# Kernel tuning notes

Hardware: AMD Instinct MI355X
Metric: run time of the kernel (lower is better)

Reference implementation:

```python
import jax, jax.numpy as jnp
import numpy as np

N_POINTS = 2_000_000
N_VOXELS = 1_500_000
N_SP = 50_000
C = 32
LN_EPS = 1e-5  # torch nn.LayerNorm default


def setup_inputs() -> dict:
    key = jax.random.key(0)
    ks = jax.random.split(key, 8)
    voxel_feats = jax.random.normal(ks[0], (N_VOXELS, C), jnp.float32)
    xyz = jax.random.normal(ks[1], (N_POINTS, 3), jnp.float32)
    p2v_map = jax.random.randint(ks[2], (N_POINTS,), 0, N_VOXELS, dtype=jnp.int32)
    sp_ids = jax.random.randint(ks[3], (N_POINTS,), 0, N_SP, dtype=jnp.int32)
    W1 = jax.random.normal(ks[4], (3, C), jnp.float32) * (1.0 / np.sqrt(3.0))
    b1 = jnp.zeros((C,), jnp.float32)
    gamma = jnp.ones((C,), jnp.float32)
    beta = jnp.zeros((C,), jnp.float32)
    W2 = jax.random.normal(ks[5], (C, C), jnp.float32) * (1.0 / np.sqrt(C))
    b2 = jnp.zeros((C,), jnp.float32)
    return {
        'voxel_feats': voxel_feats, 'xyz': xyz,
        'W1': W1, 'b1': b1, 'gamma': gamma, 'beta': beta, 'W2': W2, 'b2': b2,
        'p2v_map': p2v_map, 'sp_ids': sp_ids, 'num_superpoints': N_SP,
    }


def reference(voxel_feats, xyz, W1, b1, gamma, beta, W2, b2, p2v_map, sp_ids, num_superpoints):
    # gather voxel features to points: x = voxel_feats[p2v_map]  [N_pts, C]
    x = voxel_feats[p2v_map]

    # pos_encode MLP: Linear(3,32) -> LayerNorm(32) -> ReLU -> Linear(32,32)
    h = xyz @ W1 + b1
    mu = jnp.mean(h, axis=-1, keepdims=True)
    var = jnp.mean(jnp.square(h - mu), axis=-1, keepdims=True)
    h = (h - mu) * jax.lax.rsqrt(var + LN_EPS) * gamma + beta
    x_pos = jax.nn.relu(h) @ W2 + b2

    # scatter(reduce='mean') into superpoints; compute counts once
    counts = jax.ops.segment_sum(jnp.ones((xyz.shape[0],), x.dtype), sp_ids,
                                 num_segments=num_superpoints)
    denom = jnp.maximum(counts, 1.0)[:, None]

    def smean(v):
        return jax.ops.segment_sum(v, sp_ids, num_segments=num_superpoints) / denom

    x_sp = smean(x) + smean(x_pos)          # [S, C]
    sp_xyz = smean(xyz)                      # [S, 3]
    return (x_sp, sp_xyz)
```

## Files before the change

kernel.cpp:

```cpp
#include <hip/hip_runtime.h>
#include <hip/hip_bf16.h>

#define C 32
#define LN_EPS 1e-5f
#define P 8
#define SCAN_BLK 1024

__global__ __launch_bounds__(256) void k1_hist_rank(
    const int* __restrict__ sp_ids, int* __restrict__ count,
    int* __restrict__ rank, int n)
{
    int p = blockIdx.x * 256 + threadIdx.x;
    if (p >= n) return;
    int sp = sp_ids[p];
    rank[p] = atomicAdd(&count[sp], 1);
}

__global__ __launch_bounds__(SCAN_BLK) void k2a_scan_block(
    const int* __restrict__ count, int* __restrict__ off,
    int* __restrict__ bsum, int S)
{
    __shared__ int lds[SCAN_BLK];
    int t = threadIdx.x;
    int i = blockIdx.x * SCAN_BLK + t;
    int v = (i < S) ? count[i] : 0;
    lds[t] = v;
    __syncthreads();
    for (int d = 1; d < SCAN_BLK; d <<= 1) {
        int add = (t >= d) ? lds[t - d] : 0;
        __syncthreads();
        lds[t] += add;
        __syncthreads();
    }
    int incl = lds[t];
    if (i < S) off[i] = incl - v;
    if (t == SCAN_BLK - 1) bsum[blockIdx.x] = incl;
}

__global__ __launch_bounds__(64) void k2b_scan_bsums(int* __restrict__ bsum, int nb)
{
    int lane = threadIdx.x;
    int v = (lane < nb) ? bsum[lane] : 0;
    int own = v;
    for (int d = 1; d < 64; d <<= 1) {
        int u = __shfl_up(v, d, 64);
        if (lane >= d) v += u;
    }
    if (lane < nb) bsum[lane] = v - own;
}

__global__ __launch_bounds__(256) void k2c_add_prefix(
    int* __restrict__ off, const int* __restrict__ bsum, int S)
{
    int i = blockIdx.x * 256 + threadIdx.x;
    if (i >= S) return;
    off[i] += bsum[i / SCAN_BLK];
}

__global__ __launch_bounds__(256) void kA_mlp_scatter(
    const float* __restrict__ voxel_feats,
    const float* __restrict__ xyz,
    const float* __restrict__ W1, const float* __restrict__ b1,
    const float* __restrict__ gamma, const float* __restrict__ beta,
    const float* __restrict__ W2, const float* __restrict__ b2,
    const int* __restrict__ p2v, const int* __restrict__ sp_ids,
    const int* __restrict__ rank, const int* __restrict__ off,
    unsigned int* __restrict__ y_s,
    float* __restrict__ xyz_s,
    int n)
{
    int p = blockIdx.x * 256 + threadIdx.x;
    if (p >= n) return;

    float x0 = xyz[3 * p + 0];
    float x1 = xyz[3 * p + 1];
    float x2 = xyz[3 * p + 2];
    int v  = p2v[p];
    int sp = sp_ids[p];
    int j  = off[sp] + rank[p];

    float h[C];
    #pragma unroll
    for (int c = 0; c < C; ++c)
        h[c] = fmaf(x0, W1[c], fmaf(x1, W1[C + c], fmaf(x2, W1[2 * C + c], b1[c])));

    float s = 0.f, s2 = 0.f;
    #pragma unroll
    for (int c = 0; c < C; ++c) { s += h[c]; s2 += h[c] * h[c]; }
    float mu   = s * (1.0f / C);
    float var  = fmaf(-mu, mu, s2 * (1.0f / C));
    float rstd = rsqrtf(var + LN_EPS);

    #pragma unroll
    for (int c = 0; c < C; ++c)
        h[c] = fmaxf(fmaf((h[c] - mu) * rstd, gamma[c], beta[c]), 0.0f);

    float acc[C];
    const float4* vf4 = (const float4*)(voxel_feats + (size_t)v * C);
    #pragma unroll
    for (int q = 0; q < 8; ++q) {
        float4 f = vf4[q];
        acc[4 * q + 0] = b2[4 * q + 0] + f.x;
        acc[4 * q + 1] = b2[4 * q + 1] + f.y;
        acc[4 * q + 2] = b2[4 * q + 2] + f.z;
        acc[4 * q + 3] = b2[4 * q + 3] + f.w;
    }
    #pragma unroll
    for (int k = 0; k < C; ++k) {
        float rk = h[k];
        #pragma unroll
        for (int c = 0; c < C; ++c)
            acc[c] = fmaf(rk, W2[k * C + c], acc[c]);
    }

    unsigned int w[16];
    #pragma unroll
    for (int q = 0; q < 16; ++q) {
        __hip_bfloat162 bb = __float22bfloat162_rn(make_float2(acc[2 * q], acc[2 * q + 1]));
        w[q] = *reinterpret_cast<unsigned int*>(&bb);
    }
    uint4* dst = (uint4*)(y_s + (size_t)j * 16);
    dst[0] = make_uint4(w[0], w[1], w[2], w[3]);
    dst[1] = make_uint4(w[4], w[5], w[6], w[7]);
    dst[2] = make_uint4(w[8], w[9], w[10], w[11]);
    dst[3] = make_uint4(w[12], w[13], w[14], w[15]);

    float* xd = xyz_s + (size_t)j * 3;
    xd[0] = x0; xd[1] = x1; xd[2] = x2;
}

__global__ __launch_bounds__(256) void kB_reduce(
    const unsigned int* __restrict__ y_s,
    const float* __restrict__ xyz_s,
    const int* __restrict__ off, const int* __restrict__ count,
    float* __restrict__ out_x,
    float* __restrict__ out_xyz,
    int S)
{
    int gt  = blockIdx.x * 256 + threadIdx.x;
    int sp  = gt >> 3;
    int sub = gt & 7;
    if (sp >= S) return;

    int n    = count[sp];
    int base = off[sp];

    float acc[C];
    #pragma unroll
    for (int c = 0; c < C; ++c) acc[c] = 0.f;
    float ax = 0.f, ay = 0.f, az = 0.f;

    for (int i = sub; i < n; i += P) {
        const uint4* r4 = (const uint4*)(y_s + (size_t)(base + i) * 16);
        unsigned int w[16];
        *(uint4*)(w + 0)  = r4[0];
        *(uint4*)(w + 4)  = r4[1];
        *(uint4*)(w + 8)  = r4[2];
        *(uint4*)(w + 12) = r4[3];
        #pragma unroll
        for (int q = 0; q < 16; ++q) {
            acc[2 * q + 0] += __uint_as_float(w[q] << 16);
            acc[2 * q + 1] += __uint_as_float(w[q] & 0xFFFF0000u);
        }
        const float* xp = xyz_s + (size_t)(base + i) * 3;
        ax += xp[0]; ay += xp[1]; az += xp[2];
    }

    #pragma unroll
    for (int c = 0; c < C; ++c) {
        acc[c] += __shfl_xor(acc[c], 1);
        acc[c] += __shfl_xor(acc[c], 2);
        acc[c] += __shfl_xor(acc[c], 4);
    }
    ax += __shfl_xor(ax, 1); ax += __shfl_xor(ax, 2); ax += __shfl_xor(ax, 4);
    ay += __shfl_xor(ay, 1); ay += __shfl_xor(ay, 2); ay += __shfl_xor(ay, 4);
    az += __shfl_xor(az, 1); az += __shfl_xor(az, 2); az += __shfl_xor(az, 4);

    if (sub == 0) {
        float inv = 1.0f / fmaxf((float)n, 1.0f);
        float4* o4 = (float4*)(out_x + (size_t)sp * C);
        #pragma unroll
        for (int q = 0; q < 8; ++q) {
            float4 f;
            f.x = acc[4 * q + 0] * inv;
            f.y = acc[4 * q + 1] * inv;
            f.z = acc[4 * q + 2] * inv;
            f.w = acc[4 * q + 3] * inv;
            o4[q] = f;
        }
        out_xyz[3 * sp + 0] = ax * inv;
        out_xyz[3 * sp + 1] = ay * inv;
        out_xyz[3 * sp + 2] = az * inv;
    }
}

__global__ __launch_bounds__(256) void k3_reorder(
    const int* __restrict__ sp_ids, const int* __restrict__ rank,
    const int* __restrict__ off, int* __restrict__ order, int n)
{
    int p = blockIdx.x * 256 + threadIdx.x;
    if (p >= n) return;
    int sp = sp_ids[p];
    order[off[sp] + rank[p]] = p;
}

__global__ __launch_bounds__(256) void k4_segment_mlp_mean(
    const float* __restrict__ voxel_feats, const float* __restrict__ xyz,
    const float* __restrict__ W1, const float* __restrict__ b1,
    const float* __restrict__ gamma, const float* __restrict__ beta,
    const float* __restrict__ W2, const float* __restrict__ b2,
    const int* __restrict__ p2v, const int* __restrict__ order,
    const int* __restrict__ off, const int* __restrict__ count,
    float* __restrict__ out_x, float* __restrict__ out_xyz, int S)
{
    int gt  = blockIdx.x * 256 + threadIdx.x;
    int sp  = gt >> 3;
    int sub = gt & 7;
    if (sp >= S) return;

    int n    = count[sp];
    int base = off[sp];

    float acc[C];
    #pragma unroll
    for (int c = 0; c < C; ++c) acc[c] = 0.f;
    float ax = 0.f, ay = 0.f, az = 0.f;
    int my_pts = 0;

    for (int i = sub; i < n; i += P) {
        int p = order[base + i];
        float x0 = xyz[3 * p + 0];
        float x1 = xyz[3 * p + 1];
        float x2 = xyz[3 * p + 2];
        int v = p2v[p];

        float h[C];
        #pragma unroll
        for (int c = 0; c < C; ++c)
            h[c] = fmaf(x0, W1[c], fmaf(x1, W1[C + c], fmaf(x2, W1[2 * C + c], b1[c])));
        float s = 0.f, s2 = 0.f;
        #pragma unroll
        for (int c = 0; c < C; ++c) { s += h[c]; s2 += h[c] * h[c]; }
        float mu   = s * (1.0f / C);
        float var  = fmaf(-mu, mu, s2 * (1.0f / C));
        float rstd = rsqrtf(var + LN_EPS);
        #pragma unroll
        for (int c = 0; c < C; ++c)
            h[c] = fmaxf(fmaf((h[c] - mu) * rstd, gamma[c], beta[c]), 0.0f);

        const float4* vf4 = (const float4*)(voxel_feats + (size_t)v * C);
        #pragma unroll
        for (int q = 0; q < 8; ++q) {
            float4 f = vf4[q];
            acc[4 * q + 0] += f.x;
            acc[4 * q + 1] += f.y;
            acc[4 * q + 2] += f.z;
            acc[4 * q + 3] += f.w;
        }
        #pragma unroll
        for (int k = 0; k < C; ++k) {
            float rk = h[k];
            #pragma unroll
            for (int c = 0; c < C; ++c)
                acc[c] = fmaf(rk, W2[k * C + c], acc[c]);
        }
        ax += x0; ay += x1; az += x2;
        ++my_pts;
    }

    float fpts = (float)my_pts;
    #pragma unroll
    for (int c = 0; c < C; ++c) acc[c] = fmaf(fpts, b2[c], acc[c]);

    #pragma unroll
    for (int c = 0; c < C; ++c) {
        acc[c] += __shfl_xor(acc[c], 1);
        acc[c] += __shfl_xor(acc[c], 2);
        acc[c] += __shfl_xor(acc[c], 4);
    }
    ax += __shfl_xor(ax, 1); ax += __shfl_xor(ax, 2); ax += __shfl_xor(ax, 4);
    ay += __shfl_xor(ay, 1); ay += __shfl_xor(ay, 2); ay += __shfl_xor(ay, 4);
    az += __shfl_xor(az, 1); az += __shfl_xor(az, 2); az += __shfl_xor(az, 4);

    if (sub == 0) {
        float inv = 1.0f / fmaxf((float)n, 1.0f);
        float4* o4 = (float4*)(out_x + (size_t)sp * C);
        #pragma unroll
        for (int q = 0; q < 8; ++q) {
            float4 f;
            f.x = acc[4 * q + 0] * inv;
            f.y = acc[4 * q + 1] * inv;
            f.z = acc[4 * q + 2] * inv;
            f.w = acc[4 * q + 3] * inv;
            o4[q] = f;
        }
        out_xyz[3 * sp + 0] = ax * inv;
        out_xyz[3 * sp + 1] = ay * inv;
        out_xyz[3 * sp + 2] = az * inv;
    }
}

extern "C" void kernel_launch(void* const* d_in, const int* in_sizes, int n_in,
                              void* d_out, int out_size, void* d_ws, size_t ws_size,
                              hipStream_t stream)
{
    const float* voxel_feats = (const float*)d_in[0];
    const float* xyz         = (const float*)d_in[1];
    const float* W1          = (const float*)d_in[2];
    const float* b1          = (const float*)d_in[3];
    const float* gamma       = (const float*)d_in[4];
    const float* beta        = (const float*)d_in[5];
    const float* W2          = (const float*)d_in[6];
    const float* b2          = (const float*)d_in[7];
    const int*   p2v         = (const int*)d_in[8];
    const int*   sp_ids      = (const int*)d_in[9];

    const int n_pts = in_sizes[8];
    const int S     = out_size / 35;

    float* out_x   = (float*)d_out;
    float* out_xyz = out_x + (size_t)S * C;

    int* count = (int*)d_ws;
    int* off   = count + S;
    int* bsum  = off + S;
    int* rank  = bsum + 64;

    size_t head_bytes = ((size_t)2 * S + 64 + (size_t)n_pts) * sizeof(int);
    size_t needA = head_bytes + (size_t)n_pts * 64 + (size_t)n_pts * 12;

    int blk = 256;
    int gpts = (n_pts + blk - 1) / blk;
    int nb = (S + SCAN_BLK - 1) / SCAN_BLK;

    hipMemsetAsync(count, 0, (size_t)S * sizeof(int), stream);
    k1_hist_rank<<<gpts, blk, 0, stream>>>(sp_ids, count, rank, n_pts);
    k2a_scan_block<<<nb, SCAN_BLK, 0, stream>>>(count, off, bsum, S);
    k2b_scan_bsums<<<1, 64, 0, stream>>>(bsum, nb);
    k2c_add_prefix<<<(S + blk - 1) / blk, blk, 0, stream>>>(off, bsum, S);

    int n_thr = S * P;
    if (ws_size >= needA) {
        unsigned int* y_s = (unsigned int*)((char*)d_ws + head_bytes);
        float* xyz_s = (float*)((char*)d_ws + head_bytes + (size_t)n_pts * 64);

        kA_mlp_scatter<<<gpts, blk, 0, stream>>>(
            voxel_feats, xyz, W1, b1, gamma, beta, W2, b2,
            p2v, sp_ids, rank, off, y_s, xyz_s, n_pts);
        kB_reduce<<<(n_thr + blk - 1) / blk, blk, 0, stream>>>(
            y_s, xyz_s, off, count, out_x, out_xyz, S);
    } else {
        int* order = rank + n_pts;
        k3_reorder<<<gpts, blk, 0, stream>>>(sp_ids, rank, off, order, n_pts);
        k4_segment_mlp_mean<<<(n_thr + blk - 1) / blk, blk, 0, stream>>>(
            voxel_feats, xyz, W1, b1, gamma, beta, W2, b2,
            p2v, order, off, count, out_x, out_xyz, S);
    }
}
```

Baseline: 578.9 us.

## Pre-convert voxel features to bf16 and pack per-point records into aligned 128B slots

Adds a fused histogram/rank kernel that also converts voxel features to bf16 into workspace, so the per-point MLP kernel gathers half-size voxel rows. Per-point outputs and xyz are packed into one 128-byte aligned record, and each thread processes two points. The intent is to cut gather traffic and get full-line aligned writes. The trade-off is an extra full pass over the voxel table, zero padding that adds write bytes, and extra bf16 rounding of the input features.

```diff
diff --git a/kernel.cpp b/kernel.cpp
--- a/kernel.cpp
+++ b/kernel.cpp
@@ -5,6 +5,34 @@
 #define LN_EPS 1e-5f
 #define P 8
 #define SCAN_BLK 1024
+
+__device__ __forceinline__ unsigned pack_bf16x2(float a, float b) {
+    __hip_bfloat162 bb = __float22bfloat162_rn(make_float2(a, b));
+    return *reinterpret_cast<unsigned*>(&bb);
+}
+
+__global__ __launch_bounds__(256) void kVk1(
+    const int* __restrict__ sp_ids, int* __restrict__ count, int* __restrict__ rank,
+    const float* __restrict__ vf, unsigned* __restrict__ vf16,
+    int n_pts, int n_chunk)
+{
+    int t = blockIdx.x * 256 + threadIdx.x;
+    if (t < n_pts) {
+        int sp = sp_ids[t];
+        rank[t] = atomicAdd(&count[sp], 1);
+    }
+    if (t < n_chunk) {
+        const float4* src = (const float4*)vf + (size_t)t * 4;
+        float4 a = src[0], b = src[1], c = src[2], d = src[3];
+        uint4 o0, o1;
+        o0.x = pack_bf16x2(a.x, a.y); o0.y = pack_bf16x2(a.z, a.w);
+        o0.z = pack_bf16x2(b.x, b.y); o0.w = pack_bf16x2(b.z, b.w);
+        o1.x = pack_bf16x2(c.x, c.y); o1.y = pack_bf16x2(c.z, c.w);
+        o1.z = pack_bf16x2(d.x, d.y); o1.w = pack_bf16x2(d.z, d.w);
+        uint4* dst = (uint4*)vf16 + (size_t)t * 2;
+        dst[0] = o0; dst[1] = o1;
+    }
+}
 
 __global__ __launch_bounds__(256) void k1_hist_rank(
     const int* __restrict__ sp_ids, int* __restrict__ count,
@@ -57,85 +85,97 @@
     off[i] += bsum[i / SCAN_BLK];
 }
 
-__global__ __launch_bounds__(256) void kA_mlp_scatter(
-    const float* __restrict__ voxel_feats,
+template<bool BF16VF>
+__global__ __launch_bounds__(256) void kA_rec(
+    const void* __restrict__ vfeats,
     const float* __restrict__ xyz,
     const float* __restrict__ W1, const float* __restrict__ b1,
     const float* __restrict__ gamma, const float* __restrict__ beta,
     const float* __restrict__ W2, const float* __restrict__ b2,
     const int* __restrict__ p2v, const int* __restrict__ sp_ids,
     const int* __restrict__ rank, const int* __restrict__ off,
-    unsigned int* __restrict__ y_s,
-    float* __restrict__ xyz_s,
-    int n)
-{
-    int p = blockIdx.x * 256 + threadIdx.x;
-    if (p >= n) return;
-
-    float x0 = xyz[3 * p + 0];
-    float x1 = xyz[3 * p + 1];
-    float x2 = xyz[3 * p + 2];
-    int v  = p2v[p];
-    int sp = sp_ids[p];
-    int j  = off[sp] + rank[p];
-
-    float h[C];
-    #pragma unroll
-    for (int c = 0; c < C; ++c)
-        h[c] = fmaf(x0, W1[c], fmaf(x1, W1[C + c], fmaf(x2, W1[2 * C + c], b1[c])));
-
-    float s = 0.f, s2 = 0.f;
-    #pragma unroll
-    for (int c = 0; c < C; ++c) { s += h[c]; s2 += h[c] * h[c]; }
-    float mu   = s * (1.0f / C);
-    float var  = fmaf(-mu, mu, s2 * (1.0f / C));
-    float rstd = rsqrtf(var + LN_EPS);
-
-    #pragma unroll
-    for (int c = 0; c < C; ++c)
-        h[c] = fmaxf(fmaf((h[c] - mu) * rstd, gamma[c], beta[c]), 0.0f);
-
-    float acc[C];
-    const float4* vf4 = (const float4*)(voxel_feats + (size_t)v * C);
-    #pragma unroll
-    for (int q = 0; q < 8; ++q) {
-        float4 f = vf4[q];
-        acc[4 * q + 0] = b2[4 * q + 0] + f.x;
-        acc[4 * q + 1] = b2[4 * q + 1] + f.y;
-        acc[4 * q + 2] = b2[4 * q + 2] + f.z;
-        acc[4 * q + 3] = b2[4 * q + 3] + f.w;
-    }
-    #pragma unroll
-    for (int k = 0; k < C; ++k) {
-        float rk = h[k];
+    uint4* __restrict__ recs, int n, int half)
+{
+    int t0 = blockIdx.x * 256 + threadIdx.x;
+    #pragma unroll
+    for (int u = 0; u < 2; ++u) {
+        int p = t0 + u * half;
+        if (p >= n) continue;
+
+        float x0 = xyz[3 * p + 0];
+        float x1 = xyz[3 * p + 1];
+        float x2 = xyz[3 * p + 2];
+        int v  = p2v[p];
+        int sp = sp_ids[p];
+        int j  = off[sp] + rank[p];
+
+        float h[C];
         #pragma unroll
         for (int c = 0; c < C; ++c)
-            acc[c] = fmaf(rk, W2[k * C + c], acc[c]);
-    }
-
-    unsigned int w[16];
-    #pragma unroll
-    for (int q = 0; q < 16; ++q) {
-        __hip_bfloat162 bb = __float22bfloat162_rn(make_float2(acc[2 * q], acc[2 * q + 1]));
-        w[q] = *reinterpret_cast<unsigned int*>(&bb);
-    }
-    uint4* dst = (uint4*)(y_s + (size_t)j * 16);
-    dst[0] = make_uint4(w[0], w[1], w[2], w[3]);
-    dst[1] = make_uint4(w[4], w[5], w[6], w[7]);
-    dst[2] = make_uint4(w[8], w[9], w[10], w[11]);
-    dst[3] = make_uint4(w[12], w[13], w[14], w[15]);
-
-    float* xd = xyz_s + (size_t)j * 3;
-    xd[0] = x0; xd[1] = x1; xd[2] = x2;
-}
-
-__global__ __launch_bounds__(256) void kB_reduce(
-    const unsigned int* __restrict__ y_s,
-    const float* __restrict__ xyz_s,
+            h[c] = fmaf(x0, W1[c], fmaf(x1, W1[C + c], fmaf(x2, W1[2 * C + c], b1[c])));
+
+        float s = 0.f, s2 = 0.f;
+        #pragma unroll
+        for (int c = 0; c < C; ++c) { s += h[c]; s2 += h[c] * h[c]; }
+        float mu   = s * (1.0f / C);
+        float var  = fmaf(-mu, mu, s2 * (1.0f / C));
+        float rstd = rsqrtf(var + LN_EPS);
+        #pragma unroll
+        for (int c = 0; c < C; ++c)
+            h[c] = fmaxf(fmaf((h[c] - mu) * rstd, gamma[c], beta[c]), 0.0f);
+
+        float acc[C];
+        if (BF16VF) {
+            const uint4* g4 = (const uint4*)vfeats + (size_t)v * 4;
+            uint4 g0 = g4[0], g1 = g4[1], g2 = g4[2], g3 = g4[3];
+            unsigned gw[16] = { g0.x, g0.y, g0.z, g0.w, g1.x, g1.y, g1.z, g1.w,
+                                g2.x, g2.y, g2.z, g2.w, g3.x, g3.y, g3.z, g3.w };
+            #pragma unroll
+            for (int q = 0; q < 16; ++q) {
+                acc[2 * q + 0] = b2[2 * q + 0] + __uint_as_float(gw[q] << 16);
+                acc[2 * q + 1] = b2[2 * q + 1] + __uint_as_float(gw[q] & 0xFFFF0000u);
+            }
+        } else {
+            const float4* vf4 = (const float4*)((const float*)vfeats + (size_t)v * C);
+            #pragma unroll
+            for (int q = 0; q < 8; ++q) {
+                float4 f = vf4[q];
+                acc[4 * q + 0] = b2[4 * q + 0] + f.x;
+                acc[4 * q + 1] = b2[4 * q + 1] + f.y;
+                acc[4 * q + 2] = b2[4 * q + 2] + f.z;
+                acc[4 * q + 3] = b2[4 * q + 3] + f.w;
+            }
+        }
+
+        #pragma unroll
+        for (int k = 0; k < C; ++k) {
+            float rk = h[k];
+            #pragma unroll
+            for (int c = 0; c < C; ++c)
+                acc[c] = fmaf(rk, W2[k * C + c], acc[c]);
+        }
+
+        uint4* r = recs + (size_t)j * 8;
+        uint4 y0, y1, y2, y3;
+        y0.x = pack_bf16x2(acc[0],  acc[1]);  y0.y = pack_bf16x2(acc[2],  acc[3]);
+        y0.z = pack_bf16x2(acc[4],  acc[5]);  y0.w = pack_bf16x2(acc[6],  acc[7]);
+        y1.x = pack_bf16x2(acc[8],  acc[9]);  y1.y = pack_bf16x2(acc[10], acc[11]);
+        y1.z = pack_bf16x2(acc[12], acc[13]); y1.w = pack_bf16x2(acc[14], acc[15]);
+        y2.x = pack_bf16x2(acc[16], acc[17]); y2.y = pack_bf16x2(acc[18], acc[19]);
+        y2.z = pack_bf16x2(acc[20], acc[21]); y2.w = pack_bf16x2(acc[22], acc[23]);
+        y3.x = pack_bf16x2(acc[24], acc[25]); y3.y = pack_bf16x2(acc[26], acc[27]);
+        y3.z = pack_bf16x2(acc[28], acc[29]); y3.w = pack_bf16x2(acc[30], acc[31]);
+        r[0] = y0; r[1] = y1; r[2] = y2; r[3] = y3;
+        r[4] = make_uint4(__float_as_uint(x0), __float_as_uint(x1), __float_as_uint(x2), 0u);
+        uint4 z = make_uint4(0u, 0u, 0u, 0u);
+        r[5] = z; r[6] = z; r[7] = z;
+    }
+}
+
+__global__ __launch_bounds__(256) void kB_rec(
+    const uint4* __restrict__ recs,
     const int* __restrict__ off, const int* __restrict__ count,
-    float* __restrict__ out_x,
-    float* __restrict__ out_xyz,
-    int S)
+    float* __restrict__ out_x, float* __restrict__ out_xyz, int S)
 {
     int gt  = blockIdx.x * 256 + threadIdx.x;
     int sp  = gt >> 3;
@@ -151,19 +191,18 @@
     float ax = 0.f, ay = 0.f, az = 0.f;
 
     for (int i = sub; i < n; i += P) {
-        const uint4* r4 = (const uint4*)(y_s + (size_t)(base + i) * 16);
-        unsigned int w[16];
-        *(uint4*)(w + 0)  = r4[0];
-        *(uint4*)(w + 4)  = r4[1];
-        *(uint4*)(w + 8)  = r4[2];
-        *(uint4*)(w + 12) = r4[3];
+        const uint4* r = recs + (size_t)(base + i) * 8;
+        uint4 a = r[0], b = r[1], c4 = r[2], d = r[3], e = r[4];
+        unsigned w[16] = { a.x, a.y, a.z, a.w, b.x, b.y, b.z, b.w,
+                           c4.x, c4.y, c4.z, c4.w, d.x, d.y, d.z, d.w };
         #pragma unroll
         for (int q = 0; q < 16; ++q) {
             acc[2 * q + 0] += __uint_as_float(w[q] << 16);
             acc[2 * q + 1] += __uint_as_float(w[q] & 0xFFFF0000u);
         }
-        const float* xp = xyz_s + (size_t)(base + i) * 3;
-        ax += xp[0]; ay += xp[1]; az += xp[2];
+        ax += __uint_as_float(e.x);
+        ay += __uint_as_float(e.y);
+        az += __uint_as_float(e.z);
     }
 
     #pragma unroll
@@ -194,84 +233,88 @@
     }
 }
 
-__global__ __launch_bounds__(256) void k3_reorder(
-    const int* __restrict__ sp_ids, const int* __restrict__ rank,
-    const int* __restrict__ off, int* __restrict__ order, int n)
-{
-    int p = blockIdx.x * 256 + threadIdx.x;
-    if (p >= n) return;
-    int sp = sp_ids[p];
-    order[off[sp] + rank[p]] = p;
-}
-
-__global__ __launch_bounds__(256) void k4_segment_mlp_mean(
+__global__ __launch_bounds__(256) void kA_mlp_scatter(
     const float* __restrict__ voxel_feats, const float* __restrict__ xyz,
     const float* __restrict__ W1, const float* __restrict__ b1,
     const float* __restrict__ gamma, const float* __restrict__ beta,
     const float* __restrict__ W2, const float* __restrict__ b2,
-    const int* __restrict__ p2v, const int* __restrict__ order,
+    const int* __restrict__ p2v, const int* __restrict__ sp_ids,
+    const int* __restrict__ rank, const int* __restrict__ off,
+    unsigned int* __restrict__ y_s, float* __restrict__ xyz_s, int n)
+{
+    int p = blockIdx.x * 256 + threadIdx.x;
+    if (p >= n) return;
+    float x0 = xyz[3 * p + 0], x1 = xyz[3 * p + 1], x2 = xyz[3 * p + 2];
+    int v = p2v[p], sp = sp_ids[p];
+    int j = off[sp] + rank[p];
+    float h[C];
+    #pragma unroll
+    for (int c = 0; c < C; ++c)
+        h[c] = fmaf(x0, W1[c], fmaf(x1, W1[C + c], fmaf(x2, W1[2 * C + c], b1[c])));
+    float s = 0.f, s2 = 0.f;
+    #pragma unroll
+    for (int c = 0; c < C; ++c) { s += h[c]; s2 += h[c] * h[c]; }
+    float mu = s * (1.0f / C);
+    float var = fmaf(-mu, mu, s2 * (1.0f / C));
+    float rstd = rsqrtf(var + LN_EPS);
+    #pragma unroll
+    for (int c = 0; c < C; ++c)
+        h[c] = fmaxf(fmaf((h[c] - mu) * rstd, gamma[c], beta[c]), 0.0f);
+    float acc[C];
+    const float4* vf4 = (const float4*)(voxel_feats + (size_t)v * C);
+    #pragma unroll
+    for (int q = 0; q < 8; ++q) {
+        float4 f = vf4[q];
+        acc[4 * q + 0] = b2[4 * q + 0] + f.x;
+        acc[4 * q + 1] = b2[4 * q + 1] + f.y;
+        acc[4 * q + 2] = b2[4 * q + 2] + f.z;
+        acc[4 * q + 3] = b2[4 * q + 3] + f.w;
+    }
+    #pragma unroll
+    for (int k = 0; k < C; ++k) {
+        float rk = h[k];
+        #pragma unroll
+        for (int c = 0; c < C; ++c)
+            acc[c] = fmaf(rk, W2[k * C + c], acc[c]);
+    }
+    unsigned int w[16];
+    #pragma unroll
+    for (int q = 0; q < 16; ++q) w[q] = pack_bf16x2(acc[2 * q], acc[2 * q + 1]);
+    uint4* dst = (uint4*)(y_s + (size_t)j * 16);
+    dst[0] = make_uint4(w[0], w[1], w[2], w[3]);
+    dst[1] = make_uint4(w[4], w[5], w[6], w[7]);
+    dst[2] = make_uint4(w[8], w[9], w[10], w[11]);
+    dst[3] = make_uint4(w[12], w[13], w[14], w[15]);
+    float* xd = xyz_s + (size_t)j * 3;
+    xd[0] = x0; xd[1] = x1; xd[2] = x2;
+}
+
+__global__ __launch_bounds__(256) void kB_reduce(
+    const unsigned int* __restrict__ y_s, const float* __restrict__ xyz_s,
     const int* __restrict__ off, const int* __restrict__ count,
     float* __restrict__ out_x, float* __restrict__ out_xyz, int S)
 {
-    int gt  = blockIdx.x * 256 + threadIdx.x;
-    int sp  = gt >> 3;
-    int sub = gt & 7;
+    int gt = blockIdx.x * 256 + threadIdx.x;
+    int sp = gt >> 3, sub = gt & 7;
     if (sp >= S) return;
-
-    int n    = count[sp];
-    int base = off[sp];
-
+    int n = count[sp], base = off[sp];
     float acc[C];
     #pragma unroll
     for (int c = 0; c < C; ++c) acc[c] = 0.f;
     float ax = 0.f, ay = 0.f, az = 0.f;
-    int my_pts = 0;
-
     for (int i = sub; i < n; i += P) {
-        int p = order[base + i];
-        float x0 = xyz[3 * p + 0];
-        float x1 = xyz[3 * p + 1];
-        float x2 = xyz[3 * p + 2];
-        int v = p2v[p];
-
-        float h[C];
-        #pragma unroll
-        for (int c = 0; c < C; ++c)
-            h[c] = fmaf(x0, W1[c], fmaf(x1, W1[C + c], fmaf(x2, W1[2 * C + c], b1[c])));
-        float s = 0.f, s2 = 0.f;
-        #pragma unroll
-        for (int c = 0; c < C; ++c) { s += h[c]; s2 += h[c] * h[c]; }
-        float mu   = s * (1.0f / C);
-        float var  = fmaf(-mu, mu, s2 * (1.0f / C));
-        float rstd = rsqrtf(var + LN_EPS);
-        #pragma unroll
-        for (int c = 0; c < C; ++c)
-            h[c] = fmaxf(fmaf((h[c] - mu) * rstd, gamma[c], beta[c]), 0.0f);
-
-        const float4* vf4 = (const float4*)(voxel_feats + (size_t)v * C);
-        #pragma unroll
-        for (int q = 0; q < 8; ++q) {
-            float4 f = vf4[q];
-            acc[4 * q + 0] += f.x;
-            acc[4 * q + 1] += f.y;
-            acc[4 * q + 2] += f.z;
-            acc[4 * q + 3] += f.w;
-        }
-        #pragma unroll
-        for (int k = 0; k < C; ++k) {
-            float rk = h[k];
-            #pragma unroll
-            for (int c = 0; c < C; ++c)
-                acc[c] = fmaf(rk, W2[k * C + c], acc[c]);
-        }
-        ax += x0; ay += x1; az += x2;
-        ++my_pts;
-    }
-
-    float fpts = (float)my_pts;
-    #pragma unroll
-    for (int c = 0; c < C; ++c) acc[c] = fmaf(fpts, b2[c], acc[c]);
-
+        const uint4* r4 = (const uint4*)(y_s + (size_t)(base + i) * 16);
+        unsigned int w[16];
+        *(uint4*)(w + 0) = r4[0]; *(uint4*)(w + 4) = r4[1];
+        *(uint4*)(w + 8) = r4[2]; *(uint4*)(w + 12) = r4[3];
+        #pragma unroll
+        for (int q = 0; q < 16; ++q) {
+            acc[2 * q + 0] += __uint_as_float(w[q] << 16);
+            acc[2 * q + 1] += __uint_as_float(w[q] & 0xFFFF0000u);
+        }
+        const float* xp = xyz_s + (size_t)(base + i) * 3;
+        ax += xp[0]; ay += xp[1]; az += xp[2];
+    }
     #pragma unroll
     for (int c = 0; c < C; ++c) {
         acc[c] += __shfl_xor(acc[c], 1);
@@ -281,17 +324,14 @@
     ax += __shfl_xor(ax, 1); ax += __shfl_xor(ax, 2); ax += __shfl_xor(ax, 4);
     ay += __shfl_xor(ay, 1); ay += __shfl_xor(ay, 2); ay += __shfl_xor(ay, 4);
     az += __shfl_xor(az, 1); az += __shfl_xor(az, 2); az += __shfl_xor(az, 4);
-
     if (sub == 0) {
         float inv = 1.0f / fmaxf((float)n, 1.0f);
         float4* o4 = (float4*)(out_x + (size_t)sp * C);
         #pragma unroll
         for (int q = 0; q < 8; ++q) {
             float4 f;
-            f.x = acc[4 * q + 0] * inv;
-            f.y = acc[4 * q + 1] * inv;
-            f.z = acc[4 * q + 2] * inv;
-            f.w = acc[4 * q + 3] * inv;
+            f.x = acc[4 * q + 0] * inv; f.y = acc[4 * q + 1] * inv;
+            f.z = acc[4 * q + 2] * inv; f.w = acc[4 * q + 3] * inv;
             o4[q] = f;
         }
         out_xyz[3 * sp + 0] = ax * inv;
@@ -316,6 +356,7 @@
     const int*   sp_ids      = (const int*)d_in[9];
 
     const int n_pts = in_sizes[8];
+    const int n_vox = in_sizes[0] / C;
     const int S     = out_size / 35;
 
     float* out_x   = (float*)d_out;
@@ -326,34 +367,63 @@
     int* bsum  = off + S;
     int* rank  = bsum + 64;
 
-    size_t head_bytes = ((size_t)2 * S + 64 + (size_t)n_pts) * sizeof(int);
-    size_t needA = head_bytes + (size_t)n_pts * 64 + (size_t)n_pts * 12;
+    size_t head_b = ((size_t)2 * S + 64 + (size_t)n_pts) * sizeof(int);
+    head_b = (head_b + 255) & ~(size_t)255;
+    size_t rec_b  = (size_t)n_pts * 128;
+    size_t vf16_b = (size_t)n_vox * 64;
+
+    bool tier1 = ws_size >= head_b + rec_b + vf16_b;
+    bool tier2 = !tier1 && ws_size >= head_b + rec_b;
 
     int blk = 256;
     int gpts = (n_pts + blk - 1) / blk;
     int nb = (S + SCAN_BLK - 1) / SCAN_BLK;
+    int n_thr = S * P;
 
     hipMemsetAsync(count, 0, (size_t)S * sizeof(int), stream);
-    k1_hist_rank<<<gpts, blk, 0, stream>>>(sp_ids, count, rank, n_pts);
-    k2a_scan_block<<<nb, SCAN_BLK, 0, stream>>>(count, off, bsum, S);
-    k2b_scan_bsums<<<1, 64, 0, stream>>>(bsum, nb);
-    k2c_add_prefix<<<(S + blk - 1) / blk, blk, 0, stream>>>(off, bsum, S);
-
-    int n_thr = S * P;
-    if (ws_size >= needA) {
-        unsigned int* y_s = (unsigned int*)((char*)d_ws + head_bytes);
-        float* xyz_s = (float*)((char*)d_ws + head_bytes + (size_t)n_pts * 64);
-
+
+    if (tier1) {
+        uint4* recs = (uint4*)((char*)d_ws + head_b);
+        unsigned* vf16 = (unsigned*)((char*)d_ws + head_b + rec_b);
+        int n_chunk = n_vox * 2;
+        int gfuse = (max(n_pts, n_chunk) + blk - 1) / blk;
+
+        kVk1<<<gfuse, blk, 0, stream>>>(sp_ids, count, rank,
+                                        voxel_feats, vf16, n_pts, n_chunk);
+        k2a_scan_block<<<nb, SCAN_BLK, 0, stream>>>(count, off, bsum, S);
+        k2b_scan_bsums<<<1, 64, 0, stream>>>(bsum, nb);
+        k2c_add_prefix<<<(S + blk - 1) / blk, blk, 0, stream>>>(off, bsum, S);
+
+        int half = (n_pts + 1) / 2;
+        kA_rec<true><<<(half + blk - 1) / blk, blk, 0, stream>>>(
+            vf16, xyz, W1, b1, gamma, beta, W2, b2,
+            p2v, sp_ids, rank, off, recs, n_pts, half);
+        kB_rec<<<(n_thr + blk - 1) / blk, blk, 0, stream>>>(
+            recs, off, count, out_x, out_xyz, S);
+    } else if (tier2) {
+        uint4* recs = (uint4*)((char*)d_ws + head_b);
+        k1_hist_rank<<<gpts, blk, 0, stream>>>(sp_ids, count, rank, n_pts);
+        k2a_scan_block<<<nb, SCAN_BLK, 0, stream>>>(count, off, bsum, S);
+        k2b_scan_bsums<<<1, 64, 0, stream>>>(bsum, nb);
+        k2c_add_prefix<<<(S + blk - 1) / blk, blk, 0, stream>>>(off, bsum, S);
+
+        int half = (n_pts + 1) / 2;
+        kA_rec<false><<<(half + blk - 1) / blk, blk, 0, stream>>>(
+            voxel_feats, xyz, W1, b1, gamma, beta, W2, b2,
+            p2v, sp_ids, rank, off, recs, n_pts, half);
+        kB_rec<<<(n_thr + blk - 1) / blk, blk, 0, stream>>>(
+            recs, off, count, out_x, out_xyz, S);
+    } else {
+        unsigned int* y_s = (unsigned int*)((char*)d_ws + head_b);
+        float* xyz_s = (float*)((char*)d_ws + head_b + (size_t)n_pts * 64);
+        k1_hist_rank<<<gpts, blk, 0, stream>>>(sp_ids, count, rank, n_pts);
+        k2a_scan_block<<<nb, SCAN_BLK, 0, stream>>>(count, off, bsum, S);
+        k2b_scan_bsums<<<1, 64, 0, stream>>>(bsum, nb);
+        k2c_add_prefix<<<(S + blk - 1) / blk, blk, 0, stream>>>(off, bsum, S);
         kA_mlp_scatter<<<gpts, blk, 0, stream>>>(
             voxel_feats, xyz, W1, b1, gamma, beta, W2, b2,
             p2v, sp_ids, rank, off, y_s, xyz_s, n_pts);
         kB_reduce<<<(n_thr + blk - 1) / blk, blk, 0, stream>>>(
             y_s, xyz_s, off, count, out_x, out_xyz, S);
-    } else {
-        int* order = rank + n_pts;
-        k3_reorder<<<gpts, blk, 0, stream>>>(sp_ids, rank, off, order, n_pts);
-        k4_segment_mlp_mean<<<(n_thr + blk - 1) / blk, blk, 0, stream>>>(
-            voxel_feats, xyz, W1, b1, gamma, beta, W2, b2,
-            p2v, order, off, count, out_x, out_xyz, S);
-    }
-}
+    }
+}
```

Measured after the change: 625.1 us. +8.0%, slower.

## Fuse histogram rank into MLP kernel and gather by order in reduce

Applied to the files above, without the earlier changes.

Folds the atomic histogram/rank step into the per-point MLP kernel and writes each bf16 point row at its original index, so rows are stored contiguously instead of scattered. A separate reorder pass builds an order array. The reduce kernel then gathers rows through that order array and reads xyz directly, which drops the separate xyz scatter buffer. This removes one pass over sp_ids and the scattered 64-byte writes, but adds a reorder kernel and makes the reduce reads random.

```diff
diff --git a/kernel.cpp b/kernel.cpp
--- a/kernel.cpp
+++ b/kernel.cpp
@@ -6,14 +6,81 @@
 #define P 8
 #define SCAN_BLK 1024
 
-__global__ __launch_bounds__(256) void k1_hist_rank(
-    const int* __restrict__ sp_ids, int* __restrict__ count,
-    int* __restrict__ rank, int n)
+__device__ __forceinline__ unsigned pack_bf16x2(float a, float b) {
+    __hip_bfloat162 bb = __float22bfloat162_rn(make_float2(a, b));
+    return *reinterpret_cast<unsigned*>(&bb);
+}
+
+__global__ __launch_bounds__(256) void kA1_rank_mlp(
+    const float* __restrict__ voxel_feats,
+    const float* __restrict__ xyz,
+    const float* __restrict__ W1, const float* __restrict__ b1,
+    const float* __restrict__ gamma, const float* __restrict__ beta,
+    const float* __restrict__ W2, const float* __restrict__ b2,
+    const int* __restrict__ p2v, const int* __restrict__ sp_ids,
+    int* __restrict__ count, int* __restrict__ rank,
+    uint4* __restrict__ y_s,
+    int n)
 {
     int p = blockIdx.x * 256 + threadIdx.x;
     if (p >= n) return;
+
     int sp = sp_ids[p];
     rank[p] = atomicAdd(&count[sp], 1);
+
+    int v = p2v[p];
+    const float4* vrow = (const float4*)(voxel_feats + (size_t)v * C);
+    float4 g0 = vrow[0], g1 = vrow[1], g2 = vrow[2], g3 = vrow[3];
+    float4 g4 = vrow[4], g5 = vrow[5], g6 = vrow[6], g7 = vrow[7];
+
+    float x0 = xyz[3 * p + 0];
+    float x1 = xyz[3 * p + 1];
+    float x2 = xyz[3 * p + 2];
+
+    float h[C];
+    #pragma unroll
+    for (int c = 0; c < C; ++c)
+        h[c] = fmaf(x0, W1[c], fmaf(x1, W1[C + c], fmaf(x2, W1[2 * C + c], b1[c])));
+
+    float s = 0.f, s2 = 0.f;
+    #pragma unroll
+    for (int c = 0; c < C; ++c) { s += h[c]; s2 += h[c] * h[c]; }
+    float mu   = s * (1.0f / C);
+    float var  = fmaf(-mu, mu, s2 * (1.0f / C));
+    float rstd = rsqrtf(var + LN_EPS);
+    #pragma unroll
+    for (int c = 0; c < C; ++c)
+        h[c] = fmaxf(fmaf((h[c] - mu) * rstd, gamma[c], beta[c]), 0.0f);
+
+    float acc[C];
+    #pragma unroll
+    for (int c = 0; c < C; ++c) acc[c] = b2[c];
+    #pragma unroll
+    for (int k = 0; k < C; ++k) {
+        float rk = h[k];
+        #pragma unroll
+        for (int c = 0; c < C; ++c)
+            acc[c] = fmaf(rk, W2[k * C + c], acc[c]);
+    }
+
+    float gf[C] = { g0.x,g0.y,g0.z,g0.w, g1.x,g1.y,g1.z,g1.w,
+                    g2.x,g2.y,g2.z,g2.w, g3.x,g3.y,g3.z,g3.w,
+                    g4.x,g4.y,g4.z,g4.w, g5.x,g5.y,g5.z,g5.w,
+                    g6.x,g6.y,g6.z,g6.w, g7.x,g7.y,g7.z,g7.w };
+    #pragma unroll
+    for (int c = 0; c < C; ++c) acc[c] += gf[c];
+
+    uint4 y0, y1, y2, y3;
+    y0.x = pack_bf16x2(acc[0],  acc[1]);  y0.y = pack_bf16x2(acc[2],  acc[3]);
+    y0.z = pack_bf16x2(acc[4],  acc[5]);  y0.w = pack_bf16x2(acc[6],  acc[7]);
+    y1.x = pack_bf16x2(acc[8],  acc[9]);  y1.y = pack_bf16x2(acc[10], acc[11]);
+    y1.z = pack_bf16x2(acc[12], acc[13]); y1.w = pack_bf16x2(acc[14], acc[15]);
+    y2.x = pack_bf16x2(acc[16], acc[17]); y2.y = pack_bf16x2(acc[18], acc[19]);
+    y2.z = pack_bf16x2(acc[20], acc[21]); y2.w = pack_bf16x2(acc[22], acc[23]);
+    y3.x = pack_bf16x2(acc[24], acc[25]); y3.y = pack_bf16x2(acc[26], acc[27]);
+    y3.z = pack_bf16x2(acc[28], acc[29]); y3.w = pack_bf16x2(acc[30], acc[31]);
+    uint4* dst = y_s + (size_t)p * 4;
+    dst[0] = y0; dst[1] = y1; dst[2] = y2; dst[3] = y3;
 }
 
 __global__ __launch_bounds__(SCAN_BLK) void k2a_scan_block(
@@ -57,85 +124,22 @@
     off[i] += bsum[i / SCAN_BLK];
 }
 
-__global__ __launch_bounds__(256) void kA_mlp_scatter(
-    const float* __restrict__ voxel_feats,
-    const float* __restrict__ xyz,
-    const float* __restrict__ W1, const float* __restrict__ b1,
-    const float* __restrict__ gamma, const float* __restrict__ beta,
-    const float* __restrict__ W2, const float* __restrict__ b2,
-    const int* __restrict__ p2v, const int* __restrict__ sp_ids,
-    const int* __restrict__ rank, const int* __restrict__ off,
-    unsigned int* __restrict__ y_s,
-    float* __restrict__ xyz_s,
-    int n)
+__global__ __launch_bounds__(256) void k3_reorder(
+    const int* __restrict__ sp_ids, const int* __restrict__ rank,
+    const int* __restrict__ off, int* __restrict__ order, int n)
 {
     int p = blockIdx.x * 256 + threadIdx.x;
     if (p >= n) return;
-
-    float x0 = xyz[3 * p + 0];
-    float x1 = xyz[3 * p + 1];
-    float x2 = xyz[3 * p + 2];
-    int v  = p2v[p];
     int sp = sp_ids[p];
-    int j  = off[sp] + rank[p];
-
-    float h[C];
-    #pragma unroll
-    for (int c = 0; c < C; ++c)
-        h[c] = fmaf(x0, W1[c], fmaf(x1, W1[C + c], fmaf(x2, W1[2 * C + c], b1[c])));
-
-    float s = 0.f, s2 = 0.f;
-    #pragma unroll
-    for (int c = 0; c < C; ++c) { s += h[c]; s2 += h[c] * h[c]; }
-    float mu   = s * (1.0f / C);
-    float var  = fmaf(-mu, mu, s2 * (1.0f / C));
-    float rstd = rsqrtf(var + LN_EPS);
-
-    #pragma unroll
-    for (int c = 0; c < C; ++c)
-        h[c] = fmaxf(fmaf((h[c] - mu) * rstd, gamma[c], beta[c]), 0.0f);
-
-    float acc[C];
-    const float4* vf4 = (const float4*)(voxel_feats + (size_t)v * C);
-    #pragma unroll
-    for (int q = 0; q < 8; ++q) {
-        float4 f = vf4[q];
-        acc[4 * q + 0] = b2[4 * q + 0] + f.x;
-        acc[4 * q + 1] = b2[4 * q + 1] + f.y;
-        acc[4 * q + 2] = b2[4 * q + 2] + f.z;
-        acc[4 * q + 3] = b2[4 * q + 3] + f.w;
-    }
-    #pragma unroll
-    for (int k = 0; k < C; ++k) {
-        float rk = h[k];
-        #pragma unroll
-        for (int c = 0; c < C; ++c)
-            acc[c] = fmaf(rk, W2[k * C + c], acc[c]);
-    }
-
-    unsigned int w[16];
-    #pragma unroll
-    for (int q = 0; q < 16; ++q) {
-        __hip_bfloat162 bb = __float22bfloat162_rn(make_float2(acc[2 * q], acc[2 * q + 1]));
-        w[q] = *reinterpret_cast<unsigned int*>(&bb);
-    }
-    uint4* dst = (uint4*)(y_s + (size_t)j * 16);
-    dst[0] = make_uint4(w[0], w[1], w[2], w[3]);
-    dst[1] = make_uint4(w[4], w[5], w[6], w[7]);
-    dst[2] = make_uint4(w[8], w[9], w[10], w[11]);
-    dst[3] = make_uint4(w[12], w[13], w[14], w[15]);
-
-    float* xd = xyz_s + (size_t)j * 3;
-    xd[0] = x0; xd[1] = x1; xd[2] = x2;
-}
-
-__global__ __launch_bounds__(256) void kB_reduce(
-    const unsigned int* __restrict__ y_s,
-    const float* __restrict__ xyz_s,
+    order[off[sp] + rank[p]] = p;
+}
+
+__global__ __launch_bounds__(256) void kB_gather_reduce(
+    const uint4* __restrict__ y_s,
+    const float* __restrict__ xyz,
+    const int* __restrict__ order,
     const int* __restrict__ off, const int* __restrict__ count,
-    float* __restrict__ out_x,
-    float* __restrict__ out_xyz,
-    int S)
+    float* __restrict__ out_x, float* __restrict__ out_xyz, int S)
 {
     int gt  = blockIdx.x * 256 + threadIdx.x;
     int sp  = gt >> 3;
@@ -151,19 +155,19 @@
     float ax = 0.f, ay = 0.f, az = 0.f;
 
     for (int i = sub; i < n; i += P) {
-        const uint4* r4 = (const uint4*)(y_s + (size_t)(base + i) * 16);
-        unsigned int w[16];
-        *(uint4*)(w + 0)  = r4[0];
-        *(uint4*)(w + 4)  = r4[1];
-        *(uint4*)(w + 8)  = r4[2];
-        *(uint4*)(w + 12) = r4[3];
+        int o = order[base + i];
+        const uint4* r = y_s + (size_t)o * 4;
+        uint4 a = r[0], b = r[1], c4 = r[2], d = r[3];
+        const float* xp = xyz + 3 * (size_t)o;
+        float px = xp[0], py = xp[1], pz = xp[2];
+        unsigned w[16] = { a.x, a.y, a.z, a.w, b.x, b.y, b.z, b.w,
+                           c4.x, c4.y, c4.z, c4.w, d.x, d.y, d.z, d.w };
         #pragma unroll
         for (int q = 0; q < 16; ++q) {
             acc[2 * q + 0] += __uint_as_float(w[q] << 16);
             acc[2 * q + 1] += __uint_as_float(w[q] & 0xFFFF0000u);
         }
-        const float* xp = xyz_s + (size_t)(base + i) * 3;
-        ax += xp[0]; ay += xp[1]; az += xp[2];
+        ax += px; ay += py; az += pz;
     }
 
     #pragma unroll
@@ -194,14 +198,13 @@
     }
 }
 
-__global__ __launch_bounds__(256) void k3_reorder(
-    const int* __restrict__ sp_ids, const int* __restrict__ rank,
-    const int* __restrict__ off, int* __restrict__ order, int n)
+__global__ __launch_bounds__(256) void k1_hist_rank(
+    const int* __restrict__ sp_ids, int* __restrict__ count,
+    int* __restrict__ rank, int n)
 {
     int p = blockIdx.x * 256 + threadIdx.x;
     if (p >= n) return;
-    int sp = sp_ids[p];
-    order[off[sp] + rank[p]] = p;
+    rank[p] = atomicAdd(&count[sp_ids[p]], 1);
 }
 
 __global__ __launch_bounds__(256) void k4_segment_mlp_mean(
@@ -213,27 +216,19 @@
     const int* __restrict__ off, const int* __restrict__ count,
     float* __restrict__ out_x, float* __restrict__ out_xyz, int S)
 {
-    int gt  = blockIdx.x * 256 + threadIdx.x;
-    int sp  = gt >> 3;
-    int sub = gt & 7;
+    int gt = blockIdx.x * 256 + threadIdx.x;
+    int sp = gt >> 3, sub = gt & 7;
     if (sp >= S) return;
-
-    int n    = count[sp];
-    int base = off[sp];
-
+    int n = count[sp], base = off[sp];
     float acc[C];
     #pragma unroll
     for (int c = 0; c < C; ++c) acc[c] = 0.f;
     float ax = 0.f, ay = 0.f, az = 0.f;
     int my_pts = 0;
-
     for (int i = sub; i < n; i += P) {
         int p = order[base + i];
-        float x0 = xyz[3 * p + 0];
-        float x1 = xyz[3 * p + 1];
-        float x2 = xyz[3 * p + 2];
+        float x0 = xyz[3 * p + 0], x1 = xyz[3 * p + 1], x2 = xyz[3 * p + 2];
         int v = p2v[p];
-
         float h[C];
         #pragma unroll
         for (int c = 0; c < C; ++c)
@@ -241,21 +236,18 @@
         float s = 0.f, s2 = 0.f;
         #pragma unroll
         for (int c = 0; c < C; ++c) { s += h[c]; s2 += h[c] * h[c]; }
-        float mu   = s * (1.0f / C);
-        float var  = fmaf(-mu, mu, s2 * (1.0f / C));
+        float mu = s * (1.0f / C);
+        float var = fmaf(-mu, mu, s2 * (1.0f / C));
         float rstd = rsqrtf(var + LN_EPS);
         #pragma unroll
         for (int c = 0; c < C; ++c)
             h[c] = fmaxf(fmaf((h[c] - mu) * rstd, gamma[c], beta[c]), 0.0f);
-
         const float4* vf4 = (const float4*)(voxel_feats + (size_t)v * C);
         #pragma unroll
         for (int q = 0; q < 8; ++q) {
             float4 f = vf4[q];
-            acc[4 * q + 0] += f.x;
-            acc[4 * q + 1] += f.y;
-            acc[4 * q + 2] += f.z;
-            acc[4 * q + 3] += f.w;
+            acc[4 * q + 0] += f.x; acc[4 * q + 1] += f.y;
+            acc[4 * q + 2] += f.z; acc[4 * q + 3] += f.w;
         }
         #pragma unroll
         for (int k = 0; k < C; ++k) {
@@ -267,11 +259,9 @@
         ax += x0; ay += x1; az += x2;
         ++my_pts;
     }
-
     float fpts = (float)my_pts;
     #pragma unroll
     for (int c = 0; c < C; ++c) acc[c] = fmaf(fpts, b2[c], acc[c]);
-
     #pragma unroll
     for (int c = 0; c < C; ++c) {
         acc[c] += __shfl_xor(acc[c], 1);
@@ -281,17 +271,14 @@
     ax += __shfl_xor(ax, 1); ax += __shfl_xor(ax, 2); ax += __shfl_xor(ax, 4);
     ay += __shfl_xor(ay, 1); ay += __shfl_xor(ay, 2); ay += __shfl_xor(ay, 4);
     az += __shfl_xor(az, 1); az += __shfl_xor(az, 2); az += __shfl_xor(az, 4);
-
     if (sub == 0) {
         float inv = 1.0f / fmaxf((float)n, 1.0f);
         float4* o4 = (float4*)(out_x + (size_t)sp * C);
         #pragma unroll
         for (int q = 0; q < 8; ++q) {
             float4 f;
-            f.x = acc[4 * q + 0] * inv;
-            f.y = acc[4 * q + 1] * inv;
-            f.z = acc[4 * q + 2] * inv;
-            f.w = acc[4 * q + 3] * inv;
+            f.x = acc[4 * q + 0] * inv; f.y = acc[4 * q + 1] * inv;
+            f.z = acc[4 * q + 2] * inv; f.w = acc[4 * q + 3] * inv;
             o4[q] = f;
         }
         out_xyz[3 * sp + 0] = ax * inv;
@@ -325,32 +312,36 @@
     int* off   = count + S;
     int* bsum  = off + S;
     int* rank  = bsum + 64;
-
-    size_t head_bytes = ((size_t)2 * S + 64 + (size_t)n_pts) * sizeof(int);
-    size_t needA = head_bytes + (size_t)n_pts * 64 + (size_t)n_pts * 12;
+    int* order = rank + n_pts;
+
+    size_t head_b = ((size_t)2 * S + 64 + (size_t)2 * n_pts) * sizeof(int);
+    head_b = (head_b + 255) & ~(size_t)255;
+    size_t y_b = (size_t)n_pts * 64;
 
     int blk = 256;
     int gpts = (n_pts + blk - 1) / blk;
     int nb = (S + SCAN_BLK - 1) / SCAN_BLK;
+    int n_thr = S * P;
 
     hipMemsetAsync(count, 0, (size_t)S * sizeof(int), stream);
-    k1_hist_rank<<<gpts, blk, 0, stream>>>(sp_ids, count, rank, n_pts);
-    k2a_scan_block<<<nb, SCAN_BLK, 0, stream>>>(count, off, bsum, S);
-    k2b_scan_bsums<<<1, 64, 0, stream>>>(bsum, nb);
-    k2c_add_prefix<<<(S + blk - 1) / blk, blk, 0, stream>>>(off, bsum, S);
-
-    int n_thr = S * P;
-    if (ws_size >= needA) {
-        unsigned int* y_s = (unsigned int*)((char*)d_ws + head_bytes);
-        float* xyz_s = (float*)((char*)d_ws + head_bytes + (size_t)n_pts * 64);
-
-        kA_mlp_scatter<<<gpts, blk, 0, stream>>>(
+
+    if (ws_size >= head_b + y_b) {
+        uint4* y_s = (uint4*)((char*)d_ws + head_b);
+
+        kA1_rank_mlp<<<gpts, blk, 0, stream>>>(
             voxel_feats, xyz, W1, b1, gamma, beta, W2, b2,
-            p2v, sp_ids, rank, off, y_s, xyz_s, n_pts);
-        kB_reduce<<<(n_thr + blk - 1) / blk, blk, 0, stream>>>(
-            y_s, xyz_s, off, count, out_x, out_xyz, S);
+            p2v, sp_ids, count, rank, y_s, n_pts);
+        k2a_scan_block<<<nb, SCAN_BLK, 0, stream>>>(count, off, bsum, S);
+        k2b_scan_bsums<<<1, 64, 0, stream>>>(bsum, nb);
+        k2c_add_prefix<<<(S + blk - 1) / blk, blk, 0, stream>>>(off, bsum, S);
+        k3_reorder<<<gpts, blk, 0, stream>>>(sp_ids, rank, off, order, n_pts);
+        kB_gather_reduce<<<(n_thr + blk - 1) / blk, blk, 0, stream>>>(
+            y_s, xyz, order, off, count, out_x, out_xyz, S);
     } else {
-        int* order = rank + n_pts;
+        k1_hist_rank<<<gpts, blk, 0, stream>>>(sp_ids, count, rank, n_pts);
+        k2a_scan_block<<<nb, SCAN_BLK, 0, stream>>>(count, off, bsum, S);
+        k2b_scan_bsums<<<1, 64, 0, stream>>>(bsum, nb);
+        k2c_add_prefix<<<(S + blk - 1) / blk, blk, 0, stream>>>(off, bsum, S);
         k3_reorder<<<gpts, blk, 0, stream>>>(sp_ids, rank, off, order, n_pts);
         k4_segment_mlp_mean<<<(n_thr + blk - 1) / blk, blk, 0, stream>>>(
             voxel_feats, xyz, W1, b1, gamma, beta, W2, b2,
```

New measurement: 526.9 us. 1.1x faster.
